# Optimization experiments

Hardware: AMD Instinct MI355X
Metric: run time of the kernel (lower is better)

## Reference

```python
import jax, jax.numpy as jnp
import numpy as np

N, E, D_IN, D_H, D_OUT = 50000, 600000, 128, 128, 1


def setup_inputs() -> dict:
    key = jax.random.key(0)
    ks = jax.random.split(key, 20)
    p = lambda k, sh: jax.random.normal(k, sh, dtype=jnp.float32) * 0.05
    return {
        "x": jax.random.normal(ks[0], (N, D_IN), dtype=jnp.float32),
        "edge_weight": jax.random.uniform(ks[1], (E,), dtype=jnp.float32),
        # input LEConv (lin1: W1/b1, lin2: W2 no bias, lin3: W3/b3)
        "W1_in": p(ks[2], (D_IN, D_H)), "b1_in": jnp.zeros((D_H,), jnp.float32),
        "W2_in": p(ks[3], (D_IN, D_H)),
        "W3_in": p(ks[4], (D_IN, D_H)), "b3_in": jnp.zeros((D_H,), jnp.float32),
        # inner LEConv
        "W1_h": p(ks[5], (D_H, D_H)), "b1_h": jnp.zeros((D_H,), jnp.float32),
        "W2_h": p(ks[6], (D_H, D_H)),
        "W3_h": p(ks[7], (D_H, D_H)), "b3_h": jnp.zeros((D_H,), jnp.float32),
        # output LEConv
        "W1_o": p(ks[8], (D_H, D_OUT)), "b1_o": jnp.zeros((D_OUT,), jnp.float32),
        "W2_o": p(ks[9], (D_H, D_OUT)),
        "W3_o": p(ks[10], (D_H, D_OUT)), "b3_o": jnp.zeros((D_OUT,), jnp.float32),
        # LayerNorms
        "g1": jnp.ones((D_H,), jnp.float32), "beta1": jnp.zeros((D_H,), jnp.float32),
        "g2": jnp.ones((D_H,), jnp.float32), "beta2": jnp.zeros((D_H,), jnp.float32),
        "edge_index": jax.random.randint(ks[11], (2, E), 0, N, dtype=jnp.int32),
        "number_of_layers": 4,
    }


def _leconv(x, src, dst, w, W1, b1, W2, W3, b3):
    # PyG LEConv: out_i = lin3(x_i) + sum_{j->i} w_e * (lin1(x_j) - lin2(x_i))
    a = x @ W1 + b1                                   # [N, D_out]
    b = x @ W2                                        # [N, D_out]
    wsum = jax.ops.segment_sum(w, dst, num_segments=N)             # [N]
    agg = jax.ops.segment_sum(w[:, None] * a[src], dst, num_segments=N)  # [N, D_out]
    return agg - b * wsum[:, None] + x @ W3 + b3


def _ln(x, g, b, eps=1e-5):
    m = x.mean(-1, keepdims=True)
    v = x.var(-1, keepdims=True)
    return (x - m) * jax.lax.rsqrt(v + eps) * g + b


def reference(x, edge_weight, W1_in, b1_in, W2_in, W3_in, b3_in,
              W1_h, b1_h, W2_h, W3_h, b3_h,
              W1_o, b1_o, W2_o, W3_o, b3_o,
              g1, beta1, g2, beta2, edge_index, number_of_layers):
    src, dst = edge_index[0], edge_index[1]
    # per-feature standardization over nodes (torch std is unbiased -> ddof=1)
    x = (x - x.mean(0, keepdims=True)) / (jnp.std(x, axis=0, ddof=1, keepdims=True) + 1e-6)
    h = jax.nn.leaky_relu(
        _ln(_leconv(x, src, dst, edge_weight, W1_in, b1_in, W2_in, W3_in, b3_in), g1, beta1),
        negative_slope=0.1)
    for _ in range(number_of_layers - 2):
        h = jax.nn.leaky_relu(
            _ln(_leconv(h, src, dst, edge_weight, W1_h, b1_h, W2_h, W3_h, b3_h), g2, beta2),
            negative_slope=0.1)
    h = _leconv(h, src, dst, edge_weight, W1_o, b1_o, W2_o, W3_o, b3_o)
    return jax.nn.sigmoid(h)
```

## Files before the change

kernel.cpp:

```cpp
#include <hip/hip_runtime.h>
#include <hip/hip_bf16.h>
#include <math.h>


typedef _Float16 f16x8 __attribute__((ext_vector_type(8)));
typedef _Float16 f16x4 __attribute__((ext_vector_type(4)));
typedef float f32x4 __attribute__((ext_vector_type(4)));

#define LSTRIDE 136
#define CS_BLOCKS 512
#define WFIX 8388608.0f


__global__ __launch_bounds__(256) void prep_kernel(
    int N,
    const float* __restrict__ W1a, const float* __restrict__ W2a,
    const float* __restrict__ W3a, _Float16* __restrict__ Wta,
    const float* __restrict__ W1b, const float* __restrict__ W2b,
    const float* __restrict__ W3b, _Float16* __restrict__ Wtb,
    unsigned long long* __restrict__ degw, int* __restrict__ counter)
{
    int bid = blockIdx.x;
    int t = threadIdx.x;

    if (bid < 384) {
        int idx = bid * 256 + t;
        int set = idx >= 384 * 128;
        int id = idx - set * 384 * 128;
        int n = id >> 7, k = id & 127;
        const float* W = set ? ((n < 128) ? W1b : (n < 256) ? W2b : W3b)
                             : ((n < 128) ? W1a : (n < 256) ? W2a : W3a);
        _Float16* Wt = set ? Wtb : Wta;
        int c = n & 127;
        Wt[id] = (_Float16)W[k * 128 + c];
        return;
    }

    int idx = (bid - 384) * 256 + t;
    for (int i = idx; i < N; i += 128 * 256) degw[i] = 0ULL;
    if (idx == 0) { counter[0] = 0; counter[64] = 0; }
}


__global__ __launch_bounds__(256) void hist_cs_kernel(
    const int* __restrict__ dst, const float* __restrict__ ew,
    unsigned long long* __restrict__ degw, int* __restrict__ rank, int E,
    const float* __restrict__ x, int N,
    float* __restrict__ ps, float* __restrict__ pss)
{
    int bid = blockIdx.x;
    int t = threadIdx.x;

    if (bid >= CS_BLOCKS) {
        int e = (bid - CS_BLOCKS) * 256 + t;
        if (e < E) {
            int d = dst[e];
            unsigned int wf = __float2uint_rn(ew[e] * WFIX);
            unsigned long long old =
                atomicAdd(&degw[d], (1ULL << 32) | (unsigned long long)wf);
            rank[e] = (int)(old >> 32);
        }
        return;
    }

    __shared__ float shs[256][4];
    __shared__ float shq[256][4];
    int cb = bid;
    int g = t >> 5;
    int c = t & 31;
    const float4* xv = (const float4*)x;
    const int S = CS_BLOCKS * 8;
    float s0=0.f,s1=0.f,s2=0.f,s3=0.f, q0=0.f,q1=0.f,q2=0.f,q3=0.f;
    int r = cb * 8 + g;
    for (; r + 3*S < N; r += 4*S) {
        float4 v0 = xv[(size_t)r * 32 + c];
        float4 v1 = xv[(size_t)(r + S) * 32 + c];
        float4 v2 = xv[(size_t)(r + 2*S) * 32 + c];
        float4 v3 = xv[(size_t)(r + 3*S) * 32 + c];
        s0 += v0.x + v1.x + v2.x + v3.x;
        s1 += v0.y + v1.y + v2.y + v3.y;
        s2 += v0.z + v1.z + v2.z + v3.z;
        s3 += v0.w + v1.w + v2.w + v3.w;
        q0 += v0.x*v0.x + v1.x*v1.x + v2.x*v2.x + v3.x*v3.x;
        q1 += v0.y*v0.y + v1.y*v1.y + v2.y*v2.y + v3.y*v3.y;
        q2 += v0.z*v0.z + v1.z*v1.z + v2.z*v2.z + v3.z*v3.z;
        q3 += v0.w*v0.w + v1.w*v1.w + v2.w*v2.w + v3.w*v3.w;
    }
    for (; r < N; r += S) {
        float4 v = xv[(size_t)r * 32 + c];
        s0 += v.x; s1 += v.y; s2 += v.z; s3 += v.w;
        q0 += v.x*v.x; q1 += v.y*v.y; q2 += v.z*v.z; q3 += v.w*v.w;
    }
    shs[t][0]=s0; shs[t][1]=s1; shs[t][2]=s2; shs[t][3]=s3;
    shq[t][0]=q0; shq[t][1]=q1; shq[t][2]=q2; shq[t][3]=q3;
    __syncthreads();
    if (t < 32) {
        float S4[4] = {0,0,0,0}, Q4[4] = {0,0,0,0};
        #pragma unroll
        for (int gg = 0; gg < 8; ++gg) {
            #pragma unroll
            for (int i = 0; i < 4; ++i) {
                S4[i] += shs[t + 32*gg][i];
                Q4[i] += shq[t + 32*gg][i];
            }
        }
        #pragma unroll
        for (int i = 0; i < 4; ++i) {
            ps [cb * 128 + t*4 + i] = S4[i];
            pss[cb * 128 + t*4 + i] = Q4[i];
        }
    }
}

__global__ __launch_bounds__(256) void scan_fused_kernel(
    const unsigned long long* __restrict__ degw, int N,
    float* __restrict__ wsum, int* __restrict__ rowptr, int E,
    int* __restrict__ partial, int* __restrict__ counter)
{
    __shared__ int sh[256];
    __shared__ int lastFlag;
    __shared__ int blockOff;
    int t = threadIdx.x;
    int base = blockIdx.x * 1024 + t * 4;
    int v[4]; int s = 0;
    #pragma unroll
    for (int i = 0; i < 4; ++i) {
        int idx = base + i;
        if (idx < N) {
            unsigned long long w = degw[idx];
            v[i] = (int)(w >> 32);
            wsum[idx] = (float)(unsigned int)w * (1.0f / WFIX);
        } else v[i] = 0;
        s += v[i];
    }
    sh[t] = s; __syncthreads();
    for (int off = 1; off < 256; off <<= 1) {
        int x = sh[t];
        if (t >= off) x += sh[t - off];
        __syncthreads();
        sh[t] = x;
        __syncthreads();
    }
    if (t == 0) {
        atomicExch(&partial[blockIdx.x], sh[255]);
        __threadfence();
        int tk = atomicAdd(&counter[0], 1);
        lastFlag = (tk == (int)gridDim.x - 1) ? 1 : 0;
    }
    __syncthreads();
    if (lastFlag) {
        if (t < 64) {
            __threadfence();
            int nb = (int)gridDim.x;
            int o = (t < nb) ? atomicAdd(&partial[t], 0) : 0;
            int vv = o;
            #pragma unroll
            for (int off = 1; off < 64; off <<= 1) {
                int u = __shfl_up(vv, off, 64);
                if (t >= off) vv += u;
            }
            if (t < nb) atomicExch(&partial[t], vv - o);
        }
        __syncthreads();
        if (t == 0) { __threadfence(); atomicExch(&counter[64], 1); }
    }
    if (t == 0) {
        while (atomicAdd(&counter[64], 0) == 0) {}
        __threadfence();
        blockOff = atomicAdd(&partial[blockIdx.x], 0);
    }
    __syncthreads();
    int off0 = blockOff + ((t > 0) ? sh[t - 1] : 0);
    #pragma unroll
    for (int i = 0; i < 4; ++i) {
        int idx = base + i;
        if (idx < N) { rowptr[idx] = off0; off0 += v[i]; }
    }
    if (blockIdx.x == 0 && t == 0) rowptr[N] = E;
}

__global__ __launch_bounds__(256) void csr_fill_stats_kernel(
    const int* __restrict__ src, const int* __restrict__ dst,
    const float* __restrict__ ew, const int* __restrict__ rowptr,
    const int* __restrict__ rank, int2* __restrict__ csr, int E, int eBlocks,
    const float* __restrict__ ps, const float* __restrict__ pss, int Nn,
    float* __restrict__ mean, float* __restrict__ rstd)
{
    int bid = blockIdx.x;
    int t = threadIdx.x;
    if (bid < eBlocks) {
        int e = bid * 256 + t;
        if (e >= E) return;
        int d = dst[e];
        int pos = rowptr[d] + rank[e];
        csr[pos] = make_int2(src[e], __float_as_int(ew[e]));
        return;
    }
    __shared__ float sh1[256], sh2[256];
    int f = bid - eBlocks;
    int r0 = t * 2;
    float s1 = ps [(size_t)r0 * 128 + f] + ps [(size_t)(r0 + 1) * 128 + f];
    float s2 = pss[(size_t)r0 * 128 + f] + pss[(size_t)(r0 + 1) * 128 + f];
    sh1[t] = s1; sh2[t] = s2; __syncthreads();
    for (int off = 128; off > 0; off >>= 1) {
        if (t < off) { sh1[t] += sh1[t + off]; sh2[t] += sh2[t + off]; }
        __syncthreads();
    }
    if (t == 0) {
        float sum = sh1[0], sumsq = sh2[0];
        float m = sum / (float)Nn;
        float var = (sumsq - sum * sum / (float)Nn) / (float)(Nn - 1);
        var = fmaxf(var, 0.f);
        mean[f] = m;
        rstd[f] = 1.f / (sqrtf(var) + 1e-6f);
    }
}


__global__ __launch_bounds__(256, 2) void gemm_mfma_kernel(
    const _Float16* __restrict__ h, int N, int nTiles,
    const _Float16* __restrict__ Wt,
    const float* __restrict__ b1,
    const float* __restrict__ b3,
    const float* __restrict__ wsum,
    _Float16* __restrict__ out_a, _Float16* __restrict__ out_d)
{
    __shared__ _Float16 ldsS[64 * LSTRIDE];
    __shared__ _Float16 lds_a[64 * LSTRIDE];
    __shared__ _Float16 lds_d[64 * LSTRIDE];

    int t = threadIdx.x;
    int wave = t >> 6;
    int lane = t & 63;
    int quad = lane >> 4;
    int c16  = lane & 15;

    const f16x8* wv = (const f16x8*)Wt;
    int ntl[6] = {2*wave, 2*wave+1, 8+2*wave, 9+2*wave, 16+2*wave, 17+2*wave};
    f16x8 bfrag[6][4];
    #pragma unroll
    for (int j = 0; j < 6; ++j) {
        int nrow = ntl[j] * 16 + c16;
        #pragma unroll
        for (int s = 0; s < 4; ++s)
            bfrag[j][s] = wv[(size_t)nrow * 16 + s * 4 + quad];
    }
    float bb1[2], bb3[2];
    #pragma unroll
    for (int j = 0; j < 2; ++j) {
        int col = (2*wave + j) * 16 + c16;
        bb1[j] = b1[col];
        bb3[j] = b3[col];
    }

    const f16x8* hv = (const f16x8*)h;
    f16x8* oa = (f16x8*)out_a;
    f16x8* od = (f16x8*)out_d;

    for (int tile = blockIdx.x; tile < nTiles; tile += gridDim.x) {
        int row0 = tile * 64;

        #pragma unroll
        for (int i = 0; i < 4; ++i) {
            int idx = i * 256 + t;
            int row = idx >> 4;
            int chunk = idx & 15;
            int grow = row0 + row;
            if (grow >= N) grow = N - 1;
            *(f16x8*)&ldsS[row * LSTRIDE + chunk * 8] = hv[(size_t)grow * 16 + chunk];
        }
        __syncthreads();

        #pragma unroll
        for (int r = 0; r < 4; ++r) {
            f16x8 afrag[4];
            #pragma unroll
            for (int s = 0; s < 4; ++s)
                afrag[s] = *(const f16x8*)&ldsS[(r*16 + c16) * LSTRIDE + (s*4 + quad) * 8];

            f32x4 acc[6];
            #pragma unroll
            for (int j = 0; j < 6; ++j) acc[j] = (f32x4){0.f, 0.f, 0.f, 0.f};
            #pragma unroll
            for (int s = 0; s < 4; ++s) {
                #pragma unroll
                for (int j = 0; j < 6; ++j)
                    acc[j] = __builtin_amdgcn_mfma_f32_16x16x32_f16(afrag[s], bfrag[j][s], acc[j], 0, 0, 0);
            }

            float wsv[4];
            #pragma unroll
            for (int reg = 0; reg < 4; ++reg) {
                int gr = row0 + r*16 + quad*4 + reg;
                wsv[reg] = wsum[(gr < N) ? gr : (N - 1)];
            }
            #pragma unroll
            for (int j = 0; j < 2; ++j) {
                int col = (2*wave + j) * 16 + c16;
                #pragma unroll
                for (int reg = 0; reg < 4; ++reg) {
                    int lr = r*16 + quad*4 + reg;
                    lds_a[lr * LSTRIDE + col] = (_Float16)(acc[j][reg] + bb1[j]);
                    lds_d[lr * LSTRIDE + col] =
                        (_Float16)(acc[4+j][reg] + bb3[j] - wsv[reg] * acc[2+j][reg]);
                }
            }
        }
        __syncthreads();

        #pragma unroll
        for (int i = 0; i < 4; ++i) {
            int idx = i * 256 + t;
            int row = idx >> 4;
            int c8  = idx & 15;
            int grow = row0 + row;
            if (grow < N) {
                f16x8 va = *(const f16x8*)&lds_a[row * LSTRIDE + c8 * 8];
                oa[(size_t)grow * 16 + c8] = va;
                f16x8 vd = *(const f16x8*)&lds_d[row * LSTRIDE + c8 * 8];
                od[(size_t)grow * 16 + c8] = vd;
            }
        }
        __syncthreads();
    }
}


__global__ __launch_bounds__(256, 2) void gemm_mfma_std_kernel(
    const float* __restrict__ x,
    const float* __restrict__ meanp, const float* __restrict__ rstdp,
    int N, int nTiles,
    const _Float16* __restrict__ Wt,
    const float* __restrict__ b1,
    const float* __restrict__ b3,
    const float* __restrict__ wsum,
    _Float16* __restrict__ out_a, _Float16* __restrict__ out_d)
{
    __shared__ _Float16 ldsS[64 * LSTRIDE];
    __shared__ _Float16 lds_a[64 * LSTRIDE];
    __shared__ _Float16 lds_d[64 * LSTRIDE];

    int t = threadIdx.x;
    int wave = t >> 6;
    int lane = t & 63;
    int quad = lane >> 4;
    int c16  = lane & 15;

    const f16x8* wv = (const f16x8*)Wt;
    int ntl[6] = {2*wave, 2*wave+1, 8+2*wave, 9+2*wave, 16+2*wave, 17+2*wave};
    f16x8 bfrag[6][4];
    #pragma unroll
    for (int j = 0; j < 6; ++j) {
        int nrow = ntl[j] * 16 + c16;
        #pragma unroll
        for (int s = 0; s < 4; ++s)
            bfrag[j][s] = wv[(size_t)nrow * 16 + s * 4 + quad];
    }
    float bb1[2], bb3[2];
    #pragma unroll
    for (int j = 0; j < 2; ++j) {
        int col = (2*wave + j) * 16 + c16;
        bb1[j] = b1[col];
        bb3[j] = b3[col];
    }

    int c4 = t & 31;
    float4 mu = ((const float4*)meanp)[c4];
    float4 rs = ((const float4*)rstdp)[c4];

    const float4* xv = (const float4*)x;
    f16x8* oa = (f16x8*)out_a;
    f16x8* od = (f16x8*)out_d;

    for (int tile = blockIdx.x; tile < nTiles; tile += gridDim.x) {
        int row0 = tile * 64;

        #pragma unroll
        for (int i = 0; i < 8; ++i) {
            int idx = i * 256 + t;
            int row = idx >> 5;
            int grow = row0 + row;
            if (grow >= N) grow = N - 1;
            float4 v = xv[(size_t)grow * 32 + c4];
            f16x4 o;
            o.x = (_Float16)((v.x - mu.x) * rs.x);
            o.y = (_Float16)((v.y - mu.y) * rs.y);
            o.z = (_Float16)((v.z - mu.z) * rs.z);
            o.w = (_Float16)((v.w - mu.w) * rs.w);
            *(f16x4*)&ldsS[row * LSTRIDE + c4 * 4] = o;
        }
        __syncthreads();

        #pragma unroll
        for (int r = 0; r < 4; ++r) {
            f16x8 afrag[4];
            #pragma unroll
            for (int s = 0; s < 4; ++s)
                afrag[s] = *(const f16x8*)&ldsS[(r*16 + c16) * LSTRIDE + (s*4 + quad) * 8];

            f32x4 acc[6];
            #pragma unroll
            for (int j = 0; j < 6; ++j) acc[j] = (f32x4){0.f, 0.f, 0.f, 0.f};
            #pragma unroll
            for (int s = 0; s < 4; ++s) {
                #pragma unroll
                for (int j = 0; j < 6; ++j)
                    acc[j] = __builtin_amdgcn_mfma_f32_16x16x32_f16(afrag[s], bfrag[j][s], acc[j], 0, 0, 0);
            }

            float wsv[4];
            #pragma unroll
            for (int reg = 0; reg < 4; ++reg) {
                int gr = row0 + r*16 + quad*4 + reg;
                wsv[reg] = wsum[(gr < N) ? gr : (N - 1)];
            }
            #pragma unroll
            for (int j = 0; j < 2; ++j) {
                int col = (2*wave + j) * 16 + c16;
                #pragma unroll
                for (int reg = 0; reg < 4; ++reg) {
                    int lr = r*16 + quad*4 + reg;
                    lds_a[lr * LSTRIDE + col] = (_Float16)(acc[j][reg] + bb1[j]);
                    lds_d[lr * LSTRIDE + col] =
                        (_Float16)(acc[4+j][reg] + bb3[j] - wsv[reg] * acc[2+j][reg]);
                }
            }
        }
        __syncthreads();

        #pragma unroll
        for (int i = 0; i < 4; ++i) {
            int idx = i * 256 + t;
            int row = idx >> 4;
            int c8  = idx & 15;
            int grow = row0 + row;
            if (grow < N) {
                f16x8 va = *(const f16x8*)&lds_a[row * LSTRIDE + c8 * 8];
                oa[(size_t)grow * 16 + c8] = va;
                f16x8 vd = *(const f16x8*)&lds_d[row * LSTRIDE + c8 * 8];
                od[(size_t)grow * 16 + c8] = vd;
            }
        }
        __syncthreads();
    }
}


__global__ __launch_bounds__(256) void aggregate_ln_kernel(
    const int* __restrict__ rowptr, const int2* __restrict__ csr,
    const _Float16* __restrict__ a, const _Float16* __restrict__ d,
    const float* __restrict__ g, const float* __restrict__ beta,
    _Float16* __restrict__ out, int N)
{
    int wave = threadIdx.x >> 6;
    int lane = threadIdx.x & 63;
    int grp  = lane >> 4;
    int l    = lane & 15;
    int node = blockIdx.x * 4 + wave;
    if (node >= N) return;
    int b = rowptr[node], en = rowptr[node + 1];
    int deg = en - b;

    const f16x8* av = (const f16x8*)a;
    f16x8 dv = ((const f16x8*)d)[(size_t)node * 16 + l];
    float acc[8] = {0,0,0,0,0,0,0,0};

    int nk = (deg + 3) >> 2;
    int k = 0;
    for (; k + 4 <= nk; k += 4) {
        int2 p[4];
        #pragma unroll
        for (int j = 0; j < 4; ++j) {
            int idx = b + (k + j) * 4 + grp;
            int idc = (idx < en) ? idx : b;
            p[j] = csr[idc];
            if (idx >= en) p[j].y = 0;
        }
        f16x8 v[4];
        #pragma unroll
        for (int j = 0; j < 4; ++j)
            v[j] = av[(size_t)p[j].x * 16 + l];
        #pragma unroll
        for (int j = 0; j < 4; ++j) {
            float w = __int_as_float(p[j].y);
            #pragma unroll
            for (int i = 0; i < 8; ++i) acc[i] += w * (float)v[j][i];
        }
    }
    if (k < nk) {
        int2 p[4];
        #pragma unroll
        for (int j = 0; j < 4; ++j) {
            int idx = b + (k + j) * 4 + grp;
            int idc = (idx < en) ? idx : b;
            p[j] = csr[idc];
            if (idx >= en) p[j].y = 0;
        }
        f16x8 v[4];
        #pragma unroll
        for (int j = 0; j < 4; ++j)
            v[j] = av[(size_t)p[j].x * 16 + l];
        #pragma unroll
        for (int j = 0; j < 4; ++j) {
            float w = __int_as_float(p[j].y);
            #pragma unroll
            for (int i = 0; i < 8; ++i) acc[i] += w * (float)v[j][i];
        }
    }

    #pragma unroll
    for (int i = 0; i < 8; ++i) {
        acc[i] += __shfl_xor(acc[i], 16, 64);
        acc[i] += __shfl_xor(acc[i], 32, 64);
    }

    float v[8];
    float s = 0.f, ss = 0.f;
    #pragma unroll
    for (int i = 0; i < 8; ++i) {
        v[i] = acc[i] + (float)dv[i];
        s += v[i]; ss += v[i] * v[i];
    }
    #pragma unroll
    for (int off = 1; off <= 8; off <<= 1) {
        s  += __shfl_xor(s,  off, 64);
        ss += __shfl_xor(ss, off, 64);
    }
    float mean = s * (1.f / 128.f);
    float var = ss * (1.f / 128.f) - mean * mean;
    float rstd = rsqrtf(var + 1e-5f);

    const float4* gv4 = (const float4*)g;
    const float4* bv4 = (const float4*)beta;
    float4 ga = gv4[l*2], gb = gv4[l*2+1];
    float4 ba = bv4[l*2], bb = bv4[l*2+1];
    float go[8] = {ga.x,ga.y,ga.z,ga.w,gb.x,gb.y,gb.z,gb.w};
    float bo[8] = {ba.x,ba.y,ba.z,ba.w,bb.x,bb.y,bb.z,bb.w};
    f16x8 ov;
    #pragma unroll
    for (int i = 0; i < 8; ++i) {
        float o = (v[i] - mean) * rstd * go[i] + bo[i];
        o = o >= 0.f ? o : 0.1f * o;
        ov[i] = (_Float16)o;
    }
    if (grp == 0)
        ((f16x8*)out)[(size_t)node * 16 + l] = ov;
}


__global__ __launch_bounds__(256) void aggregate_out_kernel(
    const int* __restrict__ rowptr, const int2* __restrict__ csr,
    const _Float16* __restrict__ a, const _Float16* __restrict__ d,
    const float* __restrict__ g, const float* __restrict__ beta,
    const float* __restrict__ W1o, const float* __restrict__ b1o,
    const float* __restrict__ W2o,
    const float* __restrict__ W3o, const float* __restrict__ b3o,
    const float* __restrict__ wsum,
    float* __restrict__ a1, float* __restrict__ dpart, int N)
{
    int wave = threadIdx.x >> 6;
    int lane = threadIdx.x & 63;
    int grp  = lane >> 4;
    int l    = lane & 15;
    int node = blockIdx.x * 4 + wave;
    if (node >= N) return;
    int b = rowptr[node], en = rowptr[node + 1];
    int deg = en - b;

    const f16x8* av = (const f16x8*)a;
    f16x8 dv = ((const f16x8*)d)[(size_t)node * 16 + l];
    float wsn = wsum[node];
    float acc[8] = {0,0,0,0,0,0,0,0};

    int nk = (deg + 3) >> 2;
    int k = 0;
    for (; k + 4 <= nk; k += 4) {
        int2 p[4];
        #pragma unroll
        for (int j = 0; j < 4; ++j) {
            int idx = b + (k + j) * 4 + grp;
            int idc = (idx < en) ? idx : b;
            p[j] = csr[idc];
            if (idx >= en) p[j].y = 0;
        }
        f16x8 v[4];
        #pragma unroll
        for (int j = 0; j < 4; ++j)
            v[j] = av[(size_t)p[j].x * 16 + l];
        #pragma unroll
        for (int j = 0; j < 4; ++j) {
            float w = __int_as_float(p[j].y);
            #pragma unroll
            for (int i = 0; i < 8; ++i) acc[i] += w * (float)v[j][i];
        }
    }
    if (k < nk) {
        int2 p[4];
        #pragma unroll
        for (int j = 0; j < 4; ++j) {
            int idx = b + (k + j) * 4 + grp;
            int idc = (idx < en) ? idx : b;
            p[j] = csr[idc];
            if (idx >= en) p[j].y = 0;
        }
        f16x8 v[4];
        #pragma unroll
        for (int j = 0; j < 4; ++j)
            v[j] = av[(size_t)p[j].x * 16 + l];
        #pragma unroll
        for (int j = 0; j < 4; ++j) {
            float w = __int_as_float(p[j].y);
            #pragma unroll
            for (int i = 0; i < 8; ++i) acc[i] += w * (float)v[j][i];
        }
    }

    #pragma unroll
    for (int i = 0; i < 8; ++i) {
        acc[i] += __shfl_xor(acc[i], 16, 64);
        acc[i] += __shfl_xor(acc[i], 32, 64);
    }

    float v[8];
    float s = 0.f, ss = 0.f;
    #pragma unroll
    for (int i = 0; i < 8; ++i) {
        v[i] = acc[i] + (float)dv[i];
        s += v[i]; ss += v[i] * v[i];
    }
    #pragma unroll
    for (int off = 1; off <= 8; off <<= 1) {
        s  += __shfl_xor(s,  off, 64);
        ss += __shfl_xor(ss, off, 64);
    }
    float mean = s * (1.f / 128.f);
    float var = ss * (1.f / 128.f) - mean * mean;
    float rstd = rsqrtf(var + 1e-5f);

    const float4* gv4 = (const float4*)g;
    const float4* bv4 = (const float4*)beta;
    float4 ga = gv4[l*2], gb = gv4[l*2+1];
    float4 ba = bv4[l*2], bb = bv4[l*2+1];
    float go[8] = {ga.x,ga.y,ga.z,ga.w,gb.x,gb.y,gb.z,gb.w};
    float bo[8] = {ba.x,ba.y,ba.z,ba.w,bb.x,bb.y,bb.z,bb.w};

    float ho[8];
    #pragma unroll
    for (int i = 0; i < 8; ++i) {
        float o = (v[i] - mean) * rstd * go[i] + bo[i];
        o = o >= 0.f ? o : 0.1f * o;
        ho[i] = (float)(_Float16)o;
    }

    const float4* w1v = (const float4*)W1o;
    const float4* w2v = (const float4*)W2o;
    const float4* w3v = (const float4*)W3o;
    float4 w1a = w1v[l*2], w1b = w1v[l*2+1];
    float4 w2a = w2v[l*2], w2b = w2v[l*2+1];
    float4 w3a = w3v[l*2], w3b = w3v[l*2+1];
    float s1 = ho[0]*w1a.x + ho[1]*w1a.y + ho[2]*w1a.z + ho[3]*w1a.w
             + ho[4]*w1b.x + ho[5]*w1b.y + ho[6]*w1b.z + ho[7]*w1b.w;
    float s2 = ho[0]*w2a.x + ho[1]*w2a.y + ho[2]*w2a.z + ho[3]*w2a.w
             + ho[4]*w2b.x + ho[5]*w2b.y + ho[6]*w2b.z + ho[7]*w2b.w;
    float s3 = ho[0]*w3a.x + ho[1]*w3a.y + ho[2]*w3a.z + ho[3]*w3a.w
             + ho[4]*w3b.x + ho[5]*w3b.y + ho[6]*w3b.z + ho[7]*w3b.w;
    #pragma unroll
    for (int off = 1; off <= 8; off <<= 1) {
        s1 += __shfl_xor(s1, off, 64);
        s2 += __shfl_xor(s2, off, 64);
        s3 += __shfl_xor(s3, off, 64);
    }
    if (lane == 0) {
        a1[node] = s1 + b1o[0];
        dpart[node] = s3 + b3o[0] - wsn * s2;
    }
}


__global__ __launch_bounds__(256) void gather_out_kernel(
    const int* __restrict__ rowptr, const int2* __restrict__ csr,
    const float* __restrict__ a1, const float* __restrict__ dpart,
    float* __restrict__ out, int N)
{
    int n = blockIdx.x * 256 + threadIdx.x;
    if (n >= N) return;
    int b = rowptr[n], en = rowptr[n + 1];
    float s = dpart[n];
    int e = b;
    for (; e + 4 <= en; e += 4) {
        int2 p0 = csr[e], p1 = csr[e+1], p2 = csr[e+2], p3 = csr[e+3];
        float x0 = a1[p0.x], x1 = a1[p1.x], x2 = a1[p2.x], x3 = a1[p3.x];
        s += __int_as_float(p0.y) * x0 + __int_as_float(p1.y) * x1
           + __int_as_float(p2.y) * x2 + __int_as_float(p3.y) * x3;
    }
    for (; e < en; ++e) {
        int2 p = csr[e];
        s += __int_as_float(p.y) * a1[p.x];
    }
    out[n] = 1.f / (1.f + expf(-s));
}

extern "C" void kernel_launch(void* const* d_in, const int* in_sizes, int n_in,
                              void* d_out, int out_size, void* d_ws, size_t ws_size,
                              hipStream_t stream)
{
    const float* x     = (const float*)d_in[0];
    const float* ew    = (const float*)d_in[1];
    const float* W1_in = (const float*)d_in[2];
    const float* b1_in = (const float*)d_in[3];
    const float* W2_in = (const float*)d_in[4];
    const float* W3_in = (const float*)d_in[5];
    const float* b3_in = (const float*)d_in[6];
    const float* W1_h  = (const float*)d_in[7];
    const float* b1_h  = (const float*)d_in[8];
    const float* W2_h  = (const float*)d_in[9];
    const float* W3_h  = (const float*)d_in[10];
    const float* b3_h  = (const float*)d_in[11];
    const float* W1_o  = (const float*)d_in[12];
    const float* b1_o  = (const float*)d_in[13];
    const float* W2_o  = (const float*)d_in[14];
    const float* W3_o  = (const float*)d_in[15];
    const float* b3_o  = (const float*)d_in[16];
    const float* g1    = (const float*)d_in[17];
    const float* beta1 = (const float*)d_in[18];
    const float* g2    = (const float*)d_in[19];
    const float* beta2 = (const float*)d_in[20];
    const int*   eidx  = (const int*)d_in[21];

    const int N = in_sizes[0] / 128;
    const int E = in_sizes[1];
    const int* srcp = eidx;
    const int* dstp = eidx + E;

    size_t off = 0;
    auto carve = [&](size_t nbytes) -> void* {
        void* p = (char*)d_ws + off;
        off += (nbytes + 255) & ~(size_t)255;
        return p;
    };
    unsigned long long* degw = (unsigned long long*)carve((size_t)N * 8);
    int*      rank   = (int*)     carve((size_t)E * 4);
    _Float16* buf_h  = (_Float16*)carve((size_t)N * 128 * 2);
    _Float16* buf_a  = (_Float16*)carve((size_t)N * 128 * 2);
    _Float16* buf_d  = (_Float16*)carve((size_t)N * 128 * 2);
    int2*     csr    = (int2*)    carve((size_t)E * 8);
    _Float16* Wt_in  = (_Float16*)carve(384 * 128 * 2);
    _Float16* Wt_h   = (_Float16*)carve(384 * 128 * 2);
    int*      rowptr = (int*)     carve((size_t)(N + 1) * 4);
    int*      partial= (int*)     carve(256 * 4);
    int*      counter= (int*)     carve(256 * 4);
    float*    ps     = (float*)   carve((size_t)CS_BLOCKS * 128 * 4);
    float*    pss    = (float*)   carve((size_t)CS_BLOCKS * 128 * 4);
    float*    meanp  = (float*)   carve(128 * 4);
    float*    rstdp  = (float*)   carve(128 * 4);
    float*    wsum   = (float*)   carve((size_t)N * 4);
    float*    a1     = (float*)   carve((size_t)N * 4);
    float*    dpart  = (float*)   carve((size_t)N * 4);

    const int nodeWaveBlocks = (N + 3) / 4;
    const int eBlocks = (E + 255) / 256;
    const int nBlocks = (N + 255) / 256;
    const int nb = (N + 1023) / 1024;

    prep_kernel<<<512, 256, 0, stream>>>(
        N, W1_in, W2_in, W3_in, Wt_in, W1_h, W2_h, W3_h, Wt_h,
        degw, counter);

    hist_cs_kernel<<<CS_BLOCKS + eBlocks, 256, 0, stream>>>(
        dstp, ew, degw, rank, E, x, N, ps, pss);

    scan_fused_kernel<<<nb, 256, 0, stream>>>(degw, N, wsum, rowptr, E, partial, counter);

    csr_fill_stats_kernel<<<eBlocks + 128, 256, 0, stream>>>(
        srcp, dstp, ew, rowptr, rank, csr, E, eBlocks,
        ps, pss, N, meanp, rstdp);

    const int nTiles = (N + 63) / 64;
    const int gemmGrid = (nTiles < 512) ? nTiles : 512;

    gemm_mfma_std_kernel<<<gemmGrid, 256, 0, stream>>>(
        x, meanp, rstdp, N, nTiles, Wt_in, b1_in, b3_in, wsum, buf_a, buf_d);
    aggregate_ln_kernel<<<nodeWaveBlocks, 256, 0, stream>>>(rowptr, csr, buf_a, buf_d, g1, beta1, buf_h, N);

    gemm_mfma_kernel<<<gemmGrid, 256, 0, stream>>>(buf_h, N, nTiles, Wt_h, b1_h, b3_h, wsum, buf_a, buf_d);
    aggregate_ln_kernel<<<nodeWaveBlocks, 256, 0, stream>>>(rowptr, csr, buf_a, buf_d, g2, beta2, buf_h, N);

    gemm_mfma_kernel<<<gemmGrid, 256, 0, stream>>>(buf_h, N, nTiles, Wt_h, b1_h, b3_h, wsum, buf_a, buf_d);
    aggregate_out_kernel<<<nodeWaveBlocks, 256, 0, stream>>>(
        rowptr, csr, buf_a, buf_d, g2, beta2,
        W1_o, b1_o, W2_o, W3_o, b3_o, wsum, a1, dpart, N);

    gather_out_kernel<<<nBlocks, 256, 0, stream>>>(rowptr, csr, a1, dpart, (float*)d_out, N);
}
```

Baseline: 303.9 us.

## Regroup setup kernels: fuse CSR fill with first GEMM, stats with scan

Restructures the preprocessing pipeline by moving independent work into neighbouring launches. Weight transposition joins the histogram kernel, the feature-stat finalisation joins the degree scan, and the CSR fill runs as extra blocks of the standardized first GEMM, leaving a small zero kernel. This cuts the launch count from five to four and lets independent blocks overlap, at the cost of larger heterogeneous grids. The fused fill+GEMM kernel carries the GEMM's launch bounds and LDS footprint, which may reduce occupancy for the scatter blocks.

```diff
diff --git a/kernel.cpp b/kernel.cpp
--- a/kernel.cpp
+++ b/kernel.cpp
@@ -12,19 +12,42 @@
 #define WFIX 8388608.0f
 
 
-__global__ __launch_bounds__(256) void prep_kernel(
-    int N,
+__global__ __launch_bounds__(256) void prep_zero_kernel(
+    int N, unsigned long long* __restrict__ degw, int* __restrict__ counter)
+{
+    int idx = blockIdx.x * 256 + threadIdx.x;
+    for (int i = idx; i < N; i += 128 * 256) degw[i] = 0ULL;
+    if (idx == 0) { counter[0] = 0; counter[64] = 0; }
+}
+
+
+__global__ __launch_bounds__(256) void hist_cs_kernel(
+    const int* __restrict__ dst, const float* __restrict__ ew,
+    unsigned long long* __restrict__ degw, int* __restrict__ rank, int E,
+    const float* __restrict__ x, int N,
+    float* __restrict__ ps, float* __restrict__ pss,
     const float* __restrict__ W1a, const float* __restrict__ W2a,
     const float* __restrict__ W3a, _Float16* __restrict__ Wta,
     const float* __restrict__ W1b, const float* __restrict__ W2b,
-    const float* __restrict__ W3b, _Float16* __restrict__ Wtb,
-    unsigned long long* __restrict__ degw, int* __restrict__ counter)
+    const float* __restrict__ W3b, _Float16* __restrict__ Wtb)
 {
     int bid = blockIdx.x;
     int t = threadIdx.x;
 
-    if (bid < 384) {
-        int idx = bid * 256 + t;
+    if (bid >= CS_BLOCKS + 384) {
+        int e = (bid - CS_BLOCKS - 384) * 256 + t;
+        if (e < E) {
+            int d = dst[e];
+            unsigned int wf = __float2uint_rn(ew[e] * WFIX);
+            unsigned long long old =
+                atomicAdd(&degw[d], (1ULL << 32) | (unsigned long long)wf);
+            rank[e] = (int)(old >> 32);
+        }
+        return;
+    }
+
+    if (bid >= CS_BLOCKS) {
+        int idx = (bid - CS_BLOCKS) * 256 + t;
         int set = idx >= 384 * 128;
         int id = idx - set * 384 * 128;
         int n = id >> 7, k = id & 127;
@@ -33,33 +56,6 @@
         _Float16* Wt = set ? Wtb : Wta;
         int c = n & 127;
         Wt[id] = (_Float16)W[k * 128 + c];
-        return;
-    }
-
-    int idx = (bid - 384) * 256 + t;
-    for (int i = idx; i < N; i += 128 * 256) degw[i] = 0ULL;
-    if (idx == 0) { counter[0] = 0; counter[64] = 0; }
-}
-
-
-__global__ __launch_bounds__(256) void hist_cs_kernel(
-    const int* __restrict__ dst, const float* __restrict__ ew,
-    unsigned long long* __restrict__ degw, int* __restrict__ rank, int E,
-    const float* __restrict__ x, int N,
-    float* __restrict__ ps, float* __restrict__ pss)
-{
-    int bid = blockIdx.x;
-    int t = threadIdx.x;
-
-    if (bid >= CS_BLOCKS) {
-        int e = (bid - CS_BLOCKS) * 256 + t;
-        if (e < E) {
-            int d = dst[e];
-            unsigned int wf = __float2uint_rn(ew[e] * WFIX);
-            unsigned long long old =
-                atomicAdd(&degw[d], (1ULL << 32) | (unsigned long long)wf);
-            rank[e] = (int)(old >> 32);
-        }
         return;
     }
 
@@ -112,16 +108,43 @@
     }
 }
 
-__global__ __launch_bounds__(256) void scan_fused_kernel(
+
+__global__ __launch_bounds__(256) void scan_stats_kernel(
     const unsigned long long* __restrict__ degw, int N,
     float* __restrict__ wsum, int* __restrict__ rowptr, int E,
-    int* __restrict__ partial, int* __restrict__ counter)
-{
+    int* __restrict__ partial, int* __restrict__ counter, int nb,
+    const float* __restrict__ ps, const float* __restrict__ pss,
+    float* __restrict__ mean, float* __restrict__ rstd)
+{
+    int bid = blockIdx.x;
+    int t = threadIdx.x;
+
+    if (bid >= nb) {
+        __shared__ float sh1[256], sh2[256];
+        int f = bid - nb;
+        int r0 = t * 2;
+        float s1 = ps [(size_t)r0 * 128 + f] + ps [(size_t)(r0 + 1) * 128 + f];
+        float s2 = pss[(size_t)r0 * 128 + f] + pss[(size_t)(r0 + 1) * 128 + f];
+        sh1[t] = s1; sh2[t] = s2; __syncthreads();
+        for (int off = 128; off > 0; off >>= 1) {
+            if (t < off) { sh1[t] += sh1[t + off]; sh2[t] += sh2[t + off]; }
+            __syncthreads();
+        }
+        if (t == 0) {
+            float sum = sh1[0], sumsq = sh2[0];
+            float m = sum / (float)N;
+            float var = (sumsq - sum * sum / (float)N) / (float)(N - 1);
+            var = fmaxf(var, 0.f);
+            mean[f] = m;
+            rstd[f] = 1.f / (sqrtf(var) + 1e-6f);
+        }
+        return;
+    }
+
     __shared__ int sh[256];
     __shared__ int lastFlag;
     __shared__ int blockOff;
-    int t = threadIdx.x;
-    int base = blockIdx.x * 1024 + t * 4;
+    int base = bid * 1024 + t * 4;
     int v[4]; int s = 0;
     #pragma unroll
     for (int i = 0; i < 4; ++i) {
@@ -142,16 +165,15 @@
         __syncthreads();
     }
     if (t == 0) {
-        atomicExch(&partial[blockIdx.x], sh[255]);
+        atomicExch(&partial[bid], sh[255]);
         __threadfence();
         int tk = atomicAdd(&counter[0], 1);
-        lastFlag = (tk == (int)gridDim.x - 1) ? 1 : 0;
+        lastFlag = (tk == nb - 1) ? 1 : 0;
     }
     __syncthreads();
     if (lastFlag) {
         if (t < 64) {
             __threadfence();
-            int nb = (int)gridDim.x;
             int o = (t < nb) ? atomicAdd(&partial[t], 0) : 0;
             int vv = o;
             #pragma unroll
@@ -167,7 +189,7 @@
     if (t == 0) {
         while (atomicAdd(&counter[64], 0) == 0) {}
         __threadfence();
-        blockOff = atomicAdd(&partial[blockIdx.x], 0);
+        blockOff = atomicAdd(&partial[bid], 0);
     }
     __syncthreads();
     int off0 = blockOff + ((t > 0) ? sh[t - 1] : 0);
@@ -176,49 +198,17 @@
         int idx = base + i;
         if (idx < N) { rowptr[idx] = off0; off0 += v[i]; }
     }
-    if (blockIdx.x == 0 && t == 0) rowptr[N] = E;
-}
-
-__global__ __launch_bounds__(256) void csr_fill_stats_kernel(
+    if (bid == 0 && t == 0) rowptr[N] = E;
+}
+
+
+__global__ __launch_bounds__(256, 2) void fill_gemm1_kernel(
     const int* __restrict__ src, const int* __restrict__ dst,
     const float* __restrict__ ew, const int* __restrict__ rowptr,
     const int* __restrict__ rank, int2* __restrict__ csr, int E, int eBlocks,
-    const float* __restrict__ ps, const float* __restrict__ pss, int Nn,
-    float* __restrict__ mean, float* __restrict__ rstd)
-{
-    int bid = blockIdx.x;
-    int t = threadIdx.x;
-    if (bid < eBlocks) {
-        int e = bid * 256 + t;
-        if (e >= E) return;
-        int d = dst[e];
-        int pos = rowptr[d] + rank[e];
-        csr[pos] = make_int2(src[e], __float_as_int(ew[e]));
-        return;
-    }
-    __shared__ float sh1[256], sh2[256];
-    int f = bid - eBlocks;
-    int r0 = t * 2;
-    float s1 = ps [(size_t)r0 * 128 + f] + ps [(size_t)(r0 + 1) * 128 + f];
-    float s2 = pss[(size_t)r0 * 128 + f] + pss[(size_t)(r0 + 1) * 128 + f];
-    sh1[t] = s1; sh2[t] = s2; __syncthreads();
-    for (int off = 128; off > 0; off >>= 1) {
-        if (t < off) { sh1[t] += sh1[t + off]; sh2[t] += sh2[t + off]; }
-        __syncthreads();
-    }
-    if (t == 0) {
-        float sum = sh1[0], sumsq = sh2[0];
-        float m = sum / (float)Nn;
-        float var = (sumsq - sum * sum / (float)Nn) / (float)(Nn - 1);
-        var = fmaxf(var, 0.f);
-        mean[f] = m;
-        rstd[f] = 1.f / (sqrtf(var) + 1e-6f);
-    }
-}
-
-
-__global__ __launch_bounds__(256, 2) void gemm_mfma_kernel(
-    const _Float16* __restrict__ h, int N, int nTiles,
+    const float* __restrict__ x,
+    const float* __restrict__ meanp, const float* __restrict__ rstdp,
+    int N, int nTiles, int gemmGrid,
     const _Float16* __restrict__ Wt,
     const float* __restrict__ b1,
     const float* __restrict__ b3,
@@ -229,7 +219,19 @@
     __shared__ _Float16 lds_a[64 * LSTRIDE];
     __shared__ _Float16 lds_d[64 * LSTRIDE];
 
+    int bid = blockIdx.x;
     int t = threadIdx.x;
+
+    if (bid < eBlocks) {
+        int e = bid * 256 + t;
+        if (e < E) {
+            int d = dst[e];
+            int pos = rowptr[d] + rank[e];
+            csr[pos] = make_int2(src[e], __float_as_int(ew[e]));
+        }
+        return;
+    }
+
     int wave = t >> 6;
     int lane = t & 63;
     int quad = lane >> 4;
@@ -253,117 +255,6 @@
         bb3[j] = b3[col];
     }
 
-    const f16x8* hv = (const f16x8*)h;
-    f16x8* oa = (f16x8*)out_a;
-    f16x8* od = (f16x8*)out_d;
-
-    for (int tile = blockIdx.x; tile < nTiles; tile += gridDim.x) {
-        int row0 = tile * 64;
-
-        #pragma unroll
-        for (int i = 0; i < 4; ++i) {
-            int idx = i * 256 + t;
-            int row = idx >> 4;
-            int chunk = idx & 15;
-            int grow = row0 + row;
-            if (grow >= N) grow = N - 1;
-            *(f16x8*)&ldsS[row * LSTRIDE + chunk * 8] = hv[(size_t)grow * 16 + chunk];
-        }
-        __syncthreads();
-
-        #pragma unroll
-        for (int r = 0; r < 4; ++r) {
-            f16x8 afrag[4];
-            #pragma unroll
-            for (int s = 0; s < 4; ++s)
-                afrag[s] = *(const f16x8*)&ldsS[(r*16 + c16) * LSTRIDE + (s*4 + quad) * 8];
-
-            f32x4 acc[6];
-            #pragma unroll
-            for (int j = 0; j < 6; ++j) acc[j] = (f32x4){0.f, 0.f, 0.f, 0.f};
-            #pragma unroll
-            for (int s = 0; s < 4; ++s) {
-                #pragma unroll
-                for (int j = 0; j < 6; ++j)
-                    acc[j] = __builtin_amdgcn_mfma_f32_16x16x32_f16(afrag[s], bfrag[j][s], acc[j], 0, 0, 0);
-            }
-
-            float wsv[4];
-            #pragma unroll
-            for (int reg = 0; reg < 4; ++reg) {
-                int gr = row0 + r*16 + quad*4 + reg;
-                wsv[reg] = wsum[(gr < N) ? gr : (N - 1)];
-            }
-            #pragma unroll
-            for (int j = 0; j < 2; ++j) {
-                int col = (2*wave + j) * 16 + c16;
-                #pragma unroll
-                for (int reg = 0; reg < 4; ++reg) {
-                    int lr = r*16 + quad*4 + reg;
-                    lds_a[lr * LSTRIDE + col] = (_Float16)(acc[j][reg] + bb1[j]);
-                    lds_d[lr * LSTRIDE + col] =
-                        (_Float16)(acc[4+j][reg] + bb3[j] - wsv[reg] * acc[2+j][reg]);
-                }
-            }
-        }
-        __syncthreads();
-
-        #pragma unroll
-        for (int i = 0; i < 4; ++i) {
-            int idx = i * 256 + t;
-            int row = idx >> 4;
-            int c8  = idx & 15;
-            int grow = row0 + row;
-            if (grow < N) {
-                f16x8 va = *(const f16x8*)&lds_a[row * LSTRIDE + c8 * 8];
-                oa[(size_t)grow * 16 + c8] = va;
-                f16x8 vd = *(const f16x8*)&lds_d[row * LSTRIDE + c8 * 8];
-                od[(size_t)grow * 16 + c8] = vd;
-            }
-        }
-        __syncthreads();
-    }
-}
-
-
-__global__ __launch_bounds__(256, 2) void gemm_mfma_std_kernel(
-    const float* __restrict__ x,
-    const float* __restrict__ meanp, const float* __restrict__ rstdp,
-    int N, int nTiles,
-    const _Float16* __restrict__ Wt,
-    const float* __restrict__ b1,
-    const float* __restrict__ b3,
-    const float* __restrict__ wsum,
-    _Float16* __restrict__ out_a, _Float16* __restrict__ out_d)
-{
-    __shared__ _Float16 ldsS[64 * LSTRIDE];
-    __shared__ _Float16 lds_a[64 * LSTRIDE];
-    __shared__ _Float16 lds_d[64 * LSTRIDE];
-
-    int t = threadIdx.x;
-    int wave = t >> 6;
-    int lane = t & 63;
-    int quad = lane >> 4;
-    int c16  = lane & 15;
-
-    const f16x8* wv = (const f16x8*)Wt;
-    int ntl[6] = {2*wave, 2*wave+1, 8+2*wave, 9+2*wave, 16+2*wave, 17+2*wave};
-    f16x8 bfrag[6][4];
-    #pragma unroll
-    for (int j = 0; j < 6; ++j) {
-        int nrow = ntl[j] * 16 + c16;
-        #pragma unroll
-        for (int s = 0; s < 4; ++s)
-            bfrag[j][s] = wv[(size_t)nrow * 16 + s * 4 + quad];
-    }
-    float bb1[2], bb3[2];
-    #pragma unroll
-    for (int j = 0; j < 2; ++j) {
-        int col = (2*wave + j) * 16 + c16;
-        bb1[j] = b1[col];
-        bb3[j] = b3[col];
-    }
-
     int c4 = t & 31;
     float4 mu = ((const float4*)meanp)[c4];
     float4 rs = ((const float4*)rstdp)[c4];
@@ -372,7 +263,7 @@
     f16x8* oa = (f16x8*)out_a;
     f16x8* od = (f16x8*)out_d;
 
-    for (int tile = blockIdx.x; tile < nTiles; tile += gridDim.x) {
+    for (int tile = bid - eBlocks; tile < nTiles; tile += gemmGrid) {
         int row0 = tile * 64;
 
         #pragma unroll
@@ -388,6 +279,115 @@
             o.z = (_Float16)((v.z - mu.z) * rs.z);
             o.w = (_Float16)((v.w - mu.w) * rs.w);
             *(f16x4*)&ldsS[row * LSTRIDE + c4 * 4] = o;
+        }
+        __syncthreads();
+
+        #pragma unroll
+        for (int r = 0; r < 4; ++r) {
+            f16x8 afrag[4];
+            #pragma unroll
+            for (int s = 0; s < 4; ++s)
+                afrag[s] = *(const f16x8*)&ldsS[(r*16 + c16) * LSTRIDE + (s*4 + quad) * 8];
+
+            f32x4 acc[6];
+            #pragma unroll
+            for (int j = 0; j < 6; ++j) acc[j] = (f32x4){0.f, 0.f, 0.f, 0.f};
+            #pragma unroll
+            for (int s = 0; s < 4; ++s) {
+                #pragma unroll
+                for (int j = 0; j < 6; ++j)
+                    acc[j] = __builtin_amdgcn_mfma_f32_16x16x32_f16(afrag[s], bfrag[j][s], acc[j], 0, 0, 0);
+            }
+
+            float wsv[4];
+            #pragma unroll
+            for (int reg = 0; reg < 4; ++reg) {
+                int gr = row0 + r*16 + quad*4 + reg;
+                wsv[reg] = wsum[(gr < N) ? gr : (N - 1)];
+            }
+            #pragma unroll
+            for (int j = 0; j < 2; ++j) {
+                int col = (2*wave + j) * 16 + c16;
+                #pragma unroll
+                for (int reg = 0; reg < 4; ++reg) {
+                    int lr = r*16 + quad*4 + reg;
+                    lds_a[lr * LSTRIDE + col] = (_Float16)(acc[j][reg] + bb1[j]);
+                    lds_d[lr * LSTRIDE + col] =
+                        (_Float16)(acc[4+j][reg] + bb3[j] - wsv[reg] * acc[2+j][reg]);
+                }
+            }
+        }
+        __syncthreads();
+
+        #pragma unroll
+        for (int i = 0; i < 4; ++i) {
+            int idx = i * 256 + t;
+            int row = idx >> 4;
+            int c8  = idx & 15;
+            int grow = row0 + row;
+            if (grow < N) {
+                f16x8 va = *(const f16x8*)&lds_a[row * LSTRIDE + c8 * 8];
+                oa[(size_t)grow * 16 + c8] = va;
+                f16x8 vd = *(const f16x8*)&lds_d[row * LSTRIDE + c8 * 8];
+                od[(size_t)grow * 16 + c8] = vd;
+            }
+        }
+        __syncthreads();
+    }
+}
+
+
+__global__ __launch_bounds__(256, 2) void gemm_mfma_kernel(
+    const _Float16* __restrict__ h, int N, int nTiles,
+    const _Float16* __restrict__ Wt,
+    const float* __restrict__ b1,
+    const float* __restrict__ b3,
+    const float* __restrict__ wsum,
+    _Float16* __restrict__ out_a, _Float16* __restrict__ out_d)
+{
+    __shared__ _Float16 ldsS[64 * LSTRIDE];
+    __shared__ _Float16 lds_a[64 * LSTRIDE];
+    __shared__ _Float16 lds_d[64 * LSTRIDE];
+
+    int t = threadIdx.x;
+    int wave = t >> 6;
+    int lane = t & 63;
+    int quad = lane >> 4;
+    int c16  = lane & 15;
+
+    const f16x8* wv = (const f16x8*)Wt;
+    int ntl[6] = {2*wave, 2*wave+1, 8+2*wave, 9+2*wave, 16+2*wave, 17+2*wave};
+    f16x8 bfrag[6][4];
+    #pragma unroll
+    for (int j = 0; j < 6; ++j) {
+        int nrow = ntl[j] * 16 + c16;
+        #pragma unroll
+        for (int s = 0; s < 4; ++s)
+            bfrag[j][s] = wv[(size_t)nrow * 16 + s * 4 + quad];
+    }
+    float bb1[2], bb3[2];
+    #pragma unroll
+    for (int j = 0; j < 2; ++j) {
+        int col = (2*wave + j) * 16 + c16;
+        bb1[j] = b1[col];
+        bb3[j] = b3[col];
+    }
+
+    const f16x8* hv = (const f16x8*)h;
+    f16x8* oa = (f16x8*)out_a;
+    f16x8* od = (f16x8*)out_d;
+
+    for (int tile = blockIdx.x; tile < nTiles; tile += gridDim.x) {
+        int row0 = tile * 64;
+
+        #pragma unroll
+        for (int i = 0; i < 4; ++i) {
+            int idx = i * 256 + t;
+            int row = idx >> 4;
+            int chunk = idx & 15;
+            int grow = row0 + row;
+            if (grow >= N) grow = N - 1;
+            *(f16x8*)&ldsS[row * LSTRIDE + chunk * 8] = hv[(size_t)grow * 16 + chunk];
         }
         __syncthreads();
 
@@ -761,25 +761,24 @@
     const int eBlocks = (E + 255) / 256;
     const int nBlocks = (N + 255) / 256;
     const int nb = (N + 1023) / 1024;
-
-    prep_kernel<<<512, 256, 0, stream>>>(
-        N, W1_in, W2_in, W3_in, Wt_in, W1_h, W2_h, W3_h, Wt_h,
-        degw, counter);
-
-    hist_cs_kernel<<<CS_BLOCKS + eBlocks, 256, 0, stream>>>(
-        dstp, ew, degw, rank, E, x, N, ps, pss);
-
-    scan_fused_kernel<<<nb, 256, 0, stream>>>(degw, N, wsum, rowptr, E, partial, counter);
-
-    csr_fill_stats_kernel<<<eBlocks + 128, 256, 0, stream>>>(
-        srcp, dstp, ew, rowptr, rank, csr, E, eBlocks,
-        ps, pss, N, meanp, rstdp);
-
     const int nTiles = (N + 63) / 64;
     const int gemmGrid = (nTiles < 512) ? nTiles : 512;
 
-    gemm_mfma_std_kernel<<<gemmGrid, 256, 0, stream>>>(
-        x, meanp, rstdp, N, nTiles, Wt_in, b1_in, b3_in, wsum, buf_a, buf_d);
+    prep_zero_kernel<<<128, 256, 0, stream>>>(N, degw, counter);
+
+    hist_cs_kernel<<<CS_BLOCKS + 384 + eBlocks, 256, 0, stream>>>(
+        dstp, ew, degw, rank, E, x, N, ps, pss,
+        W1_in, W2_in, W3_in, Wt_in, W1_h, W2_h, W3_h, Wt_h);
+
+    scan_stats_kernel<<<nb + 128, 256, 0, stream>>>(
+        degw, N, wsum, rowptr, E, partial, counter, nb,
+        ps, pss, meanp, rstdp);
+
+    fill_gemm1_kernel<<<eBlocks + gemmGrid, 256, 0, stream>>>(
+        srcp, dstp, ew, rowptr, rank, csr, E, eBlocks,
+        x, meanp, rstdp, N, nTiles, gemmGrid,
+        Wt_in, b1_in, b3_in, wsum, buf_a, buf_d);
+
     aggregate_ln_kernel<<<nodeWaveBlocks, 256, 0, stream>>>(rowptr, csr, buf_a, buf_d, g1, beta1, buf_h, N);
 
     gemm_mfma_kernel<<<gemmGrid, 256, 0, stream>>>(buf_h, N, nTiles, Wt_h, b1_h, b3_h, wsum, buf_a, buf_d);
```

After: 298.9 us, median of 2. No clear change (-1.6%).
